# Kernel tuning notes

Measured on AMD Instinct MI355X. Metric: run time of the kernel, lower is better.

Reference implementation:

```python
import jax, jax.numpy as jnp
import numpy as np

N_NODES = 10000
N_EDGES = 128000


def _edge_conv(x, row, col, edge_attr, w1, b1, w2, b2):
    # gather endpoints, concat edge features, 2-layer MLP per edge
    m = jnp.concatenate([x[row], x[col], edge_attr], axis=1)  # [E, 2*in+edge]
    m = jax.nn.relu(m @ w1 + b1) @ w2 + b2                    # [E, out]
    # scatter-mean onto source nodes (flow='target_to_source' -> aggregate on row)
    n = x.shape[0]
    s = jax.ops.segment_sum(m, row, num_segments=n)
    cnt = jax.ops.segment_sum(jnp.ones((row.shape[0], 1), m.dtype), row, num_segments=n)
    out = s / jnp.maximum(cnt, 1.0)
    return out, m


def setup_inputs() -> dict:
    key = jax.random.key(0)
    ks = jax.random.split(key, 24)
    f = jnp.float32

    def lin(kw, kb, fan_in, fan_out):
        lim = 1.0 / np.sqrt(fan_in)
        w = jax.random.uniform(kw, (fan_in, fan_out), f, -lim, lim)
        b = jax.random.uniform(kb, (fan_out,), f, -lim, lim)
        return w, b

    inp = {}
    inp['x_org'] = jax.random.normal(ks[0], (N_NODES, 256), f)
    inp['x_rot'] = jax.random.normal(ks[1], (N_NODES, 4), f)
    inp['edge_index'] = jax.random.randint(ks[2], (2, N_EDGES), 0, N_NODES, jnp.int64 if jax.config.jax_enable_x64 else jnp.int32)
    inp['edge_attr'] = jax.random.normal(ks[3], (N_EDGES, 640), f)
    inp['edge_rot'] = jax.random.normal(ks[4], (N_EDGES, 4), f)

    # conv1: Linear(2*260+644=1164, 64), Linear(64, 64)
    inp['c1_w1'], inp['c1_b1'] = lin(ks[5], ks[6], 1164, 64)
    inp['c1_w2'], inp['c1_b2'] = lin(ks[7], ks[8], 64, 64)
    # conv2: Linear(2*64+704=832, 64), Linear(64, 64)
    inp['c2_w1'], inp['c2_b1'] = lin(ks[9], ks[10], 832, 64)
    inp['c2_w2'], inp['c2_b2'] = lin(ks[11], ks[12], 64, 64)
    # conv3: Linear(2*128+128=384, 64), Linear(64, 64)
    inp['c3_w1'], inp['c3_b1'] = lin(ks[13], ks[14], 384, 64)
    inp['c3_w2'], inp['c3_b2'] = lin(ks[15], ks[16], 64, 64)
    # conv4: Linear(384, 64), Linear(64, 64)
    inp['c4_w1'], inp['c4_b1'] = lin(ks[17], ks[18], 384, 64)
    inp['c4_w2'], inp['c4_b2'] = lin(ks[19], ks[20], 64, 64)
    # lin1: Linear(64, 4)
    inp['lin1_w'], inp['lin1_b'] = lin(ks[21], ks[22], 64, 4)
    # edge_fc: Linear(64, 32) -> ReLU -> Linear(32, 1)
    k23 = jax.random.split(ks[23], 4)
    inp['efc_w1'], inp['efc_b1'] = lin(k23[0], k23[1], 64, 32)
    inp['efc_w2'], inp['efc_b2'] = lin(k23[2], k23[3], 32, 1)
    return inp


def reference(x_org, x_rot, edge_index, edge_attr, edge_rot,
              c1_w1, c1_b1, c1_w2, c1_b2,
              c2_w1, c2_b1, c2_w2, c2_b2,
              c3_w1, c3_b1, c3_w2, c3_b2,
              c4_w1, c4_b1, c4_w2, c4_b2,
              lin1_w, lin1_b, efc_w1, efc_b1, efc_w2, efc_b2):
    node_feat = jnp.concatenate([x_org, x_rot], axis=1)
    edge_feat = jnp.concatenate([edge_attr, edge_rot], axis=1)
    row, col = edge_index[0], edge_index[1]
    E = edge_index.shape[1]

    x1, edge_x1 = _edge_conv(node_feat, row, col, edge_feat, c1_w1, c1_b1, c1_w2, c1_b2)
    edge_x1 = jax.nn.relu(edge_x1)

    x2, edge_x2 = _edge_conv(x1, row, col, jnp.concatenate([edge_attr, edge_x1], axis=1),
                             c2_w1, c2_b1, c2_w2, c2_b2)
    x2 = jax.nn.relu(x2)
    edge_x2 = jax.nn.relu(edge_x2)

    x3, edge_x3 = _edge_conv(jnp.concatenate([x2, x1], axis=1), row, col,
                             jnp.concatenate([edge_x2, edge_x1], axis=1),
                             c3_w1, c3_b1, c3_w2, c3_b2)
    x3 = jax.nn.relu(x3)
    edge_x3 = jax.nn.relu(edge_x3)

    x4, edge_x4 = _edge_conv(jnp.concatenate([x3, x2], axis=1), row, col,
                             jnp.concatenate([edge_x3, edge_x2], axis=1),
                             c4_w1, c4_b1, c4_w2, c4_b2)
    x4 = jax.nn.relu(x4)

    x = x4 @ lin1_w + lin1_b  # [N, 4]
    h = edge_x4[: E // 2] + edge_x4[E // 2:]
    pred_edge_res = jax.nn.relu(h @ efc_w1 + efc_b1) @ efc_w2 + efc_b2  # [E/2, 1]

    # F.normalize(x, p=2, dim=1)
    x = x / jnp.maximum(jnp.linalg.norm(x, axis=1, keepdims=True), 1e-12)
    return x, pred_edge_res
```

## Files before the change

### kernel.cpp

```cpp
#include <hip/hip_runtime.h>
#include <stdint.h>


#define N_NODES 10000
#define N_EDGES 128000
#define E_HALF  64000
#define NBLK    1000

typedef unsigned short u16;

using bf16x8 = __attribute__((ext_vector_type(8))) short;
using f32x4  = __attribute__((ext_vector_type(4))) float;

#define MFMA16(A, B, C) C = __builtin_amdgcn_mfma_f32_16x16x32_bf16(A, B, C, 0, 0, 0)

__device__ __align__(256) float g_acc[N_NODES * 64];
__device__ __align__(256) float g_deg[N_NODES];
__device__ __align__(256) float g_P[N_NODES * 128];
__device__ __align__(256) float g_x1[N_NODES * 64];
__device__ __align__(256) float g_x2[N_NODES * 64];
__device__ __align__(256) float g_x3[N_NODES * 64];
__device__ __align__(256) u16  g_fragA[(size_t)NBLK * 16384];
__device__ __align__(256) u16  g_fragB[(size_t)NBLK * 16384];
__device__ __align__(256) float g_Q2 [(size_t)N_EDGES * 64];
__device__ __align__(256) float g_ex4[(size_t)N_EDGES * 64];
__device__ __align__(256) u16  g_wpA_hi[2 * 4096];
__device__ __align__(256) u16  g_wpA_lo[2 * 4096];
__device__ __align__(256) u16  g_wp2_hi[4096];
__device__ __align__(256) u16  g_wp2_lo[4096];
__device__ __align__(256) u16  g_wnp_hi[4 * 8192];
__device__ __align__(256) u16  g_wnp_lo[4 * 8192];
__device__ __align__(256) u16  g_wpC_hi[10 * 8192];
__device__ __align__(256) u16  g_wpC_lo[10 * 8192];
__device__ __align__(256) int g_row[N_EDGES];
__device__ __align__(256) int g_col[N_EDGES];
__device__ int g_mode;
__device__ int g_is64;

__device__ __forceinline__ float b2f(u16 u) {
    return __uint_as_float(((unsigned int)u) << 16);
}
__device__ __forceinline__ u16 f2b(float f) {
    unsigned int u = __float_as_uint(f);
    u += 0x7FFFu + ((u >> 16) & 1u);
    return (u16)(u >> 16);
}
__device__ __forceinline__ float ldf(const u16* p)   { return b2f(*p); }
__device__ __forceinline__ float ldf(const float* p) { return *p; }
__device__ __forceinline__ void  stf(u16* p, float v)   { *p = f2b(v); }
__device__ __forceinline__ void  stf(float* p, float v) { *p = v; }

__device__ __forceinline__ float4 load4(const float* p) { return *(const float4*)p; }
__device__ __forceinline__ float4 load4(const u16* p) {
    ushort4 v = *(const ushort4*)p;
    return make_float4(b2f(v.x), b2f(v.y), b2f(v.z), b2f(v.w));
}

__device__ __forceinline__ void split_pack(float4 v, uint2& hi, uint2& lo) {
    unsigned int ux = __float_as_uint(v.x), uy = __float_as_uint(v.y);
    unsigned int uz = __float_as_uint(v.z), uw = __float_as_uint(v.w);
    unsigned int hx = ux & 0xFFFF0000u, hy = uy & 0xFFFF0000u;
    unsigned int hz = uz & 0xFFFF0000u, hw = uw & 0xFFFF0000u;
    hi.x = (hx >> 16) | hy;
    hi.y = (hz >> 16) | hw;
    u16 lx = f2b(v.x - __uint_as_float(hx));
    u16 ly = f2b(v.y - __uint_as_float(hy));
    u16 lz = f2b(v.z - __uint_as_float(hz));
    u16 lw = f2b(v.w - __uint_as_float(hw));
    lo.x = (unsigned int)lx | ((unsigned int)ly << 16);
    lo.y = (unsigned int)lz | ((unsigned int)lw << 16);
}

__device__ __forceinline__ void mk_frag(float4 v0, float4 v1,
                                        bf16x8& fh, bf16x8& fl) {
    uint2 h0, l0, h1, l1;
    split_pack(v0, h0, l0);
    split_pack(v1, h1, l1);
    union { unsigned int w[4]; bf16x8 v; } H, L;
    H.w[0] = h0.x; H.w[1] = h0.y; H.w[2] = h1.x; H.w[3] = h1.y;
    L.w[0] = l0.x; L.w[1] = l0.y; L.w[2] = l1.x; L.w[3] = l1.y;
    fh = H.v; fl = L.v;
}

__global__ void detect_kernel(const void* x_org_v, const int* __restrict__ eidx) {
    const u16* w = (const u16*)x_org_v;
    const int t = threadIdx.x;
    int ok = 0;
    for (int i = t; i < 128; i += 64) {
        u16 v = w[i];
        int ex = (v >> 7) & 0xFF;
        ok += ((ex >= 0x68 && ex <= 0x88) || ((v & 0x7FFFu) == 0)) ? 1 : 0;
    }
    #pragma unroll
    for (int off = 32; off >= 1; off >>= 1) ok += __shfl_xor(ok, off);
    bool allz = true;
    for (int i = t; i < 2048; i += 64) allz = allz && (eidx[2 * i + 1] == 0);
    unsigned long long m = __ballot(allz);
    if (t == 0) {
        g_mode = (ok >= 110) ? 0 : 1;
        g_is64 = (m == ~0ull) ? 1 : 0;
    }
}

__global__ void cvt_idx(const int* __restrict__ eidx) {
    const int e = blockIdx.x * 256 + threadIdx.x;
    if (g_is64) {
        g_row[e] = eidx[2 * e];
        g_col[e] = eidx[2 * (e + N_EDGES)];
    } else {
        g_row[e] = eidx[e];
        g_col[e] = eidx[e + N_EDGES];
    }
}

__global__ void zero_all() {
    const int i = blockIdx.x * 256 + threadIdx.x;
    g_acc[i] = 0.f;
    if (i < N_NODES) g_deg[i] = 0.f;
}

__global__ void deg_kernel() {
    const int e = blockIdx.x * 256 + threadIdx.x;
    if (e < N_EDGES) atomicAdd(&g_deg[g_row[e]], 1.0f);
}

template<typename TW>
__device__ void pack_w_body(const TW* w1a, const TW* w2, const TW* w1b,
                            int we, int ns, int hioff, int nsn, int nsc) {
    const int idx = blockIdx.x * 256 + threadIdx.x;
    const int t1 = ns * 4096;
    const int t2 = t1 + 4096;
    const int t3 = t2 + nsn * 8192;
    if (idx < t1) {
        const int s = idx >> 12;
        const int rem = idx & 4095;
        const int kt = rem >> 11, ct = (rem >> 9) & 3, l = (rem >> 3) & 63, r = rem & 7;
        const int k = s * 64 + kt * 32 + 4 * (l >> 4) + (r & 3) + 16 * (r >> 2);
        const float v = ldf(w1a + (size_t)(we + k) * 64 + ct * 16 + (l & 15));
        const u16 hh = f2b(v);
        g_wpA_hi[idx] = hh;
        g_wpA_lo[idx] = f2b(v - b2f(hh));
    } else if (idx < t2) {
        const int rem = idx - t1;
        const int kt = rem >> 11, ct = (rem >> 9) & 3, l = (rem >> 3) & 63, r = rem & 7;
        const int k = kt * 32 + 4 * (l >> 4) + (r & 3) + 16 * (r >> 2);
        const float v = ldf(w2 + (size_t)k * 64 + ct * 16 + (l & 15));
        const u16 hh = f2b(v);
        g_wp2_hi[rem] = hh;
        g_wp2_lo[rem] = f2b(v - b2f(hh));
    } else if (idx < t3) {
        const int rem = idx - t2;
        const int s = rem >> 13;
        const int kt = (rem >> 12) & 1, ct = (rem >> 9) & 7, l = (rem >> 3) & 63, r = rem & 7;
        const int k = s * 64 + kt * 32 + 4 * (l >> 4) + (r & 3) + 16 * (r >> 2);
        const int col = ct * 16 + (l & 15);
        const int row = (col < 64) ? k : (hioff + k);
        const float v = ldf(w1a + (size_t)row * 64 + (col & 63));
        const u16 hh = f2b(v);
        g_wnp_hi[rem] = hh;
        g_wnp_lo[rem] = f2b(v - b2f(hh));
    } else if (idx < t3 + nsc * 8192) {
        const int rem = idx - t3;
        const int s = rem >> 13;
        const int kt = (rem >> 12) & 1, ct = (rem >> 9) & 7, l = (rem >> 3) & 63, r = rem & 7;
        const int k = s * 64 + kt * 32 + 4 * (l >> 4) + (r & 3) + 16 * (r >> 2);
        const int col = ct * 16 + (l & 15);
        float v;
        if (col < 64) v = ldf(w1a + (size_t)(520 + k) * 64 + col);
        else          v = ldf(w1b + (size_t)(128 + k) * 64 + (col - 64));
        const u16 hh = f2b(v);
        g_wpC_hi[rem] = hh;
        g_wpC_lo[rem] = f2b(v - b2f(hh));
    }
}
__global__ void pack_w_k(const void* w1a, const void* w2, const void* w1b,
                         int we, int ns, int hioff, int nsn, int nsc) {
    if (g_mode == 0)
        pack_w_body<u16>((const u16*)w1a, (const u16*)w2, (const u16*)w1b,
                         we, ns, hioff, nsn, nsc);
    else
        pack_w_body<float>((const float*)w1a, (const float*)w2, (const float*)w1b,
                         we, ns, hioff, nsn, nsc);
}

template<typename TA, int NS1, int NS2, bool TAIL>
__device__ void node_mfma_body(float* smrot, float* smwt,
        const TA* A1, const float* A2, const TA* rotsrc, const TA* w1, float* P) {
    constexpr int NS = NS1 + NS2;
    const int t = threadIdx.x;
    const int lane = t & 63, wid = t >> 6;
    const int q = lane >> 4, n = lane & 15;
    const int r0b = blockIdx.x * 64;

    if constexpr (TAIL) {
        if (t < 64) {
            const int rr = min(r0b + t, N_NODES - 1);
            float4 v = load4(rotsrc + (size_t)rr * 4);
            smrot[t * 4 + 0] = v.x; smrot[t * 4 + 1] = v.y;
            smrot[t * 4 + 2] = v.z; smrot[t * 4 + 3] = v.w;
        }
        for (int i = t; i < 512; i += 256) {
            const int j = i >> 7, c = i & 127;
            const int row = (c < 64) ? (256 + j) : (516 + j);
            smwt[i] = ldf(w1 + (size_t)row * 64 + (c & 63));
        }
        __syncthreads();
    }

    const int arow = min(r0b + wid * 16 + n, N_NODES - 1);

    f32x4 acc[8];
    #pragma unroll
    for (int ct = 0; ct < 8; ++ct) acc[ct] = (f32x4){0.f, 0.f, 0.f, 0.f};

    #pragma unroll
    for (int s = 0; s < NS; ++s) {
        #pragma unroll
        for (int kt = 0; kt < 2; ++kt) {
            float4 v0, v1;
            if (s < NS1) {
                const TA* p = A1 + (size_t)arow * (NS1 * 64) + s * 64 + kt * 32 + q * 4;
                v0 = load4(p); v1 = load4(p + 16);
            } else {
                const float* p = A2 + (size_t)arow * (NS2 * 64) + (s - NS1) * 64
                               + kt * 32 + q * 4;
                v0 = load4(p); v1 = load4(p + 16);
            }
            bf16x8 ah, al;
            mk_frag(v0, v1, ah, al);
            const u16* wph = g_wnp_hi + s * 8192;
            const u16* wpl = g_wnp_lo + s * 8192;
            #pragma unroll
            for (int ct = 0; ct < 8; ++ct) {
                bf16x8 bh = *(const bf16x8*)&wph[(kt * 8 + ct) * 512 + lane * 8];
                bf16x8 bl = *(const bf16x8*)&wpl[(kt * 8 + ct) * 512 + lane * 8];
                MFMA16(ah, bh, acc[ct]);
                MFMA16(al, bh, acc[ct]);
                MFMA16(ah, bl, acc[ct]);
            }
        }
    }

    #pragma unroll
    for (int ct = 0; ct < 8; ++ct) {
        #pragma unroll
        for (int i = 0; i < 4; ++i) {
            const int rl = wid * 16 + 4 * q + i;
            const int row = r0b + rl;
            const int col = ct * 16 + n;
            float v = acc[ct][i];
            if constexpr (TAIL)
                v += smrot[rl * 4 + 0] * smwt[0 * 128 + col]
                   + smrot[rl * 4 + 1] * smwt[1 * 128 + col]
                   + smrot[rl * 4 + 2] * smwt[2 * 128 + col]
                   + smrot[rl * 4 + 3] * smwt[3 * 128 + col];
            if (row < N_NODES) P[(size_t)row * 128 + col] = v;
        }
    }
}

template<int NS1, bool TAIL>
__global__ void __launch_bounds__(256) node_mfma_in(
        const void* A1, const void* rotsrc, const void* w1, float* __restrict__ P) {
    __shared__ float smrot[256], smwt[512];
    if (g_mode == 0)
        node_mfma_body<u16, NS1, 0, TAIL>(smrot, smwt, (const u16*)A1,
            nullptr, (const u16*)rotsrc, (const u16*)w1, P);
    else
        node_mfma_body<float, NS1, 0, TAIL>(smrot, smwt, (const float*)A1,
            nullptr, (const float*)rotsrc, (const float*)w1, P);
}

template<int NS1, int NS2>
__global__ void __launch_bounds__(256) node_mfma_ws(
        const float* A1, const float* A2, float* __restrict__ P) {
    __shared__ float smrot[256], smwt[512];
    node_mfma_body<float, NS1, NS2, false>(smrot, smwt, A1, A2,
        (const float*)nullptr, (const float*)nullptr, P);
}

__device__ __forceinline__ void frag_store_o(u16* smA, int wid, int lane,
        const f32x4 (&oacc)[2][4], u16* Fdst, int blkid) {
    const int q = lane >> 4, n = lane & 15;
    #pragma unroll
    for (int rt = 0; rt < 2; ++rt)
        #pragma unroll
        for (int ct = 0; ct < 4; ++ct)
            #pragma unroll
            for (int i = 0; i < 4; ++i) {
                float v = fmaxf(oacc[rt][ct][i], 0.f);
                unsigned int hb = __float_as_uint(v) & 0xFFFF0000u;
                const u16 hh = (u16)(hb >> 16);
                const u16 hl = f2b(v - __uint_as_float(hb));
                const int off = wid * 4096
                              + (((ct >> 1) * 2 + rt) * 64 + (n >> 2) * 16 + 4 * q + i) * 8
                              + (ct & 1) * 4 + (n & 3);
                smA[off]        = hh;
                smA[off + 2048] = hl;
            }
    #pragma unroll
    for (int kt = 0; kt < 2; ++kt)
        #pragma unroll
        for (int rtl = 0; rtl < 2; ++rtl) {
            const int src = wid * 4096 + ((kt * 2 + rtl) * 64 + lane) * 8;
            bf16x8 h8 = *(const bf16x8*)&smA[src];
            bf16x8 l8 = *(const bf16x8*)&smA[src + 2048];
            const size_t gb = (size_t)blkid * 16384
                            + (size_t)(kt * 8 + wid * 2 + rtl) * 512 + lane * 8;
            *(bf16x8*)&Fdst[gb]        = h8;
            *(bf16x8*)&Fdst[gb + 8192] = l8;
        }
}

template<typename TA, typename TW>
__device__ void edge_c1_body(u16* smA, int* srow, int* scol,
        float* b1s, float* b2s, float* rot, float* wtl,
        const TA* efa, const TA* rotsrc,
        const TW* w1, const TW* b1v, const TW* b2v) {
    const int t = threadIdx.x;
    const int lane = t & 63, wid = t >> 6;
    const int q = lane >> 4, n = lane & 15;
    const int e0 = blockIdx.x * 128;

    if (t < 128) srow[t] = g_row[e0 + t];
    else         scol[t - 128] = g_col[e0 + t - 128];
    if (t >= 128 && t < 192) b1s[t - 128] = ldf(b1v + (t - 128));
    if (t >= 192)            b2s[t - 192] = ldf(b2v + (t - 192));
    if (t < 128) {
        float4 r4 = load4(rotsrc + (size_t)(e0 + t) * 4);
        rot[t * 4 + 0] = r4.x; rot[t * 4 + 1] = r4.y;
        rot[t * 4 + 2] = r4.z; rot[t * 4 + 3] = r4.w;
    }
    wtl[t] = ldf(w1 + (size_t)(1160 + (t >> 6)) * 64 + (t & 63));
    __syncthreads();

    f32x4 acc[2][8];
    #pragma unroll
    for (int a_ = 0; a_ < 2; ++a_)
        #pragma unroll
        for (int b_ = 0; b_ < 8; ++b_)
            acc[a_][b_] = (f32x4){0.f, 0.f, 0.f, 0.f};

    const TA* arow0 = efa + (size_t)(e0 + wid * 32 + n) * 640;
    const TA* arow1 = efa + (size_t)(e0 + wid * 32 + 16 + n) * 640;

    auto issue = [&](float4 (&buf)[2][2][2], int s) {
        const int cb = s * 64 + q * 4;
        #pragma unroll
        for (int kt = 0; kt < 2; ++kt) {
            buf[0][kt][0] = load4(arow0 + cb + kt * 32);
            buf[0][kt][1] = load4(arow0 + cb + kt * 32 + 16);
            buf[1][kt][0] = load4(arow1 + cb + kt * 32);
            buf[1][kt][1] = load4(arow1 + cb + kt * 32 + 16);
        }
    };
    auto step = [&](float4 (&buf)[2][2][2], int s) {
        const u16* wph = g_wpC_hi + s * 8192;
        const u16* wpl = g_wpC_lo + s * 8192;
        #pragma unroll
        for (int kt = 0; kt < 2; ++kt) {
            bf16x8 ah0, al0, ah1, al1;
            mk_frag(buf[0][kt][0], buf[0][kt][1], ah0, al0);
            mk_frag(buf[1][kt][0], buf[1][kt][1], ah1, al1);
            #pragma unroll
            for (int ct = 0; ct < 8; ++ct) {
                bf16x8 bh = *(const bf16x8*)&wph[(kt * 8 + ct) * 512 + lane * 8];
                bf16x8 bl = *(const bf16x8*)&wpl[(kt * 8 + ct) * 512 + lane * 8];
                MFMA16(ah0, bh, acc[0][ct]);
                MFMA16(ah1, bh, acc[1][ct]);
                MFMA16(al0, bh, acc[0][ct]);
                MFMA16(al1, bh, acc[1][ct]);
                MFMA16(ah0, bl, acc[0][ct]);
                MFMA16(ah1, bl, acc[1][ct]);
            }
        }
    };

    float4 bufA[2][2][2], bufB[2][2][2];
    issue(bufA, 0);
    for (int s = 0; s < 10; s += 2) {
        issue(bufB, s + 1);
        step(bufA, s);
        if (s + 2 < 10) issue(bufA, s + 2);
        step(bufB, s + 1);
    }

    #pragma unroll
    for (int rt = 0; rt < 2; ++rt)
        #pragma unroll
        for (int c2 = 0; c2 < 4; ++c2)
            #pragma unroll
            for (int i = 0; i < 4; ++i) {
                const int rl = wid * 32 + rt * 16 + 4 * q + i;
                g_Q2[(size_t)(e0 + rl) * 64 + c2 * 16 + n] = acc[rt][4 + c2][i];
            }

    #pragma unroll
    for (int rt = 0; rt < 2; ++rt)
        #pragma unroll
        for (int ct = 0; ct < 4; ++ct)
            #pragma unroll
            for (int i = 0; i < 4; ++i) {
                const int rl = wid * 32 + rt * 16 + 4 * q + i;
                const int col = ct * 16 + n;
                float v = acc[rt][ct][i] + b1s[col]
                        + g_P[(size_t)srow[rl] * 128 + col]
                        + g_P[(size_t)scol[rl] * 128 + 64 + col]
                        + rot[rl * 4 + 0] * wtl[0 * 64 + col]
                        + rot[rl * 4 + 1] * wtl[1 * 64 + col]
                        + rot[rl * 4 + 2] * wtl[2 * 64 + col]
                        + rot[rl * 4 + 3] * wtl[3 * 64 + col];
                v = fmaxf(v, 0.f);
                unsigned int hb = __float_as_uint(v) & 0xFFFF0000u;
                const u16 hh = (u16)(hb >> 16);
                const u16 hl = f2b(v - __uint_as_float(hb));
                const int off = wid * 4096
                              + (((ct >> 1) * 2 + rt) * 64 + (n >> 2) * 16 + 4 * q + i) * 8
                              + (ct & 1) * 4 + (n & 3);
                smA[off]        = hh;
                smA[off + 2048] = hl;
            }

    f32x4 oacc[2][4];
    #pragma unroll
    for (int rt = 0; rt < 2; ++rt)
        #pragma unroll
        for (int ct = 0; ct < 4; ++ct) {
            const float bb = b2s[ct * 16 + n];
            oacc[rt][ct] = (f32x4){bb, bb, bb, bb};
        }
    #pragma unroll
    for (int kt = 0; kt < 2; ++kt) {
        const int r0 = wid * 4096 + ((kt * 2 + 0) * 64 + lane) * 8;
        const int r1 = wid * 4096 + ((kt * 2 + 1) * 64 + lane) * 8;
        bf16x8 ah0 = *(const bf16x8*)&smA[r0];
        bf16x8 ah1 = *(const bf16x8*)&smA[r1];
        bf16x8 al0 = *(const bf16x8*)&smA[r0 + 2048];
        bf16x8 al1 = *(const bf16x8*)&smA[r1 + 2048];
        #pragma unroll
        for (int ct = 0; ct < 4; ++ct) {
            bf16x8 bh = *(const bf16x8*)&g_wp2_hi[(kt * 4 + ct) * 512 + lane * 8];
            bf16x8 bl = *(const bf16x8*)&g_wp2_lo[(kt * 4 + ct) * 512 + lane * 8];
            MFMA16(ah0, bh, oacc[0][ct]);
            MFMA16(ah1, bh, oacc[1][ct]);
            MFMA16(al0, bh, oacc[0][ct]);
            MFMA16(al1, bh, oacc[1][ct]);
            MFMA16(ah0, bl, oacc[0][ct]);
            MFMA16(ah1, bl, oacc[1][ct]);
        }
    }

    #pragma unroll
    for (int rt = 0; rt < 2; ++rt)
        #pragma unroll
        for (int ct = 0; ct < 4; ++ct)
            #pragma unroll
            for (int i = 0; i < 4; ++i) {
                const int rl = wid * 32 + rt * 16 + 4 * q + i;
                atomicAdd(&g_acc[(size_t)srow[rl] * 64 + ct * 16 + n], oacc[rt][ct][i]);
            }
    frag_store_o(smA, wid, lane, oacc, g_fragA, blockIdx.x);
}

__global__ void __launch_bounds__(256, 3) edge_c1(
        const void* efa, const void* rotsrc,
        const void* w1, const void* b1, const void* b2) {
    __shared__ u16 smA[16384];
    __shared__ int srow[128], scol[128];
    __shared__ float b1s[64], b2s[64], rot[512], wtl[256];
    if (g_mode == 0)
        edge_c1_body<u16, u16>(smA, srow, scol, b1s, b2s, rot, wtl,
            (const u16*)efa, (const u16*)rotsrc,
            (const u16*)w1, (const u16*)b1, (const u16*)b2);
    else
        edge_c1_body<float, float>(smA, srow, scol, b1s, b2s, rot, wtl,
            (const float*)efa, (const float*)rotsrc,
            (const float*)w1, (const float*)b1, (const float*)b2);
}

template<typename TW, int NSF, bool HASQ2, bool FRAG_OUT>
__device__ void edge_lite_body(u16* smA, int* srow, int* scol,
        float* b1s, float* b2s,
        const u16* f0, const u16* f1,
        const TW* b1v, const TW* b2v, u16* Ffrag, float* fout) {
    const int t = threadIdx.x;
    const int lane = t & 63, wid = t >> 6;
    const int q = lane >> 4, n = lane & 15;
    const int e0 = blockIdx.x * 128;
    const size_t blkb = (size_t)blockIdx.x * 16384;

    if (t < 128) srow[t] = g_row[e0 + t];
    else         scol[t - 128] = g_col[e0 + t - 128];
    if (t >= 128 && t < 192) b1s[t - 128] = ldf(b1v + (t - 128));
    if (t >= 192)            b2s[t - 192] = ldf(b2v + (t - 192));
    __syncthreads();

    f32x4 acc[2][4];
    #pragma unroll
    for (int a_ = 0; a_ < 2; ++a_)
        #pragma unroll
        for (int b_ = 0; b_ < 4; ++b_)
            acc[a_][b_] = (f32x4){0.f, 0.f, 0.f, 0.f};

    #pragma unroll
    for (int s = 0; s < NSF; ++s) {
        const u16* fs = (s == 0) ? f0 : f1;
        const u16* wph = g_wpA_hi + s * 4096;
        const u16* wpl = g_wpA_lo + s * 4096;
        #pragma unroll
        for (int kt = 0; kt < 2; ++kt) {
            const size_t ba0 = blkb + (size_t)(kt * 8 + wid * 2 + 0) * 512 + lane * 8;
            const size_t ba1 = blkb + (size_t)(kt * 8 + wid * 2 + 1) * 512 + lane * 8;
            bf16x8 ah0 = *(const bf16x8*)&fs[ba0];
            bf16x8 al0 = *(const bf16x8*)&fs[ba0 + 8192];
            bf16x8 ah1 = *(const bf16x8*)&fs[ba1];
            bf16x8 al1 = *(const bf16x8*)&fs[ba1 + 8192];
            #pragma unroll
            for (int ct = 0; ct < 4; ++ct) {
                bf16x8 bh = *(const bf16x8*)&wph[(kt * 4 + ct) * 512 + lane * 8];
                bf16x8 bl = *(const bf16x8*)&wpl[(kt * 4 + ct) * 512 + lane * 8];
                MFMA16(ah0, bh, acc[0][ct]);
                MFMA16(ah1, bh, acc[1][ct]);
                MFMA16(al0, bh, acc[0][ct]);
                MFMA16(al1, bh, acc[1][ct]);
                MFMA16(ah0, bl, acc[0][ct]);
                MFMA16(ah1, bl, acc[1][ct]);
            }
        }
    }

    #pragma unroll
    for (int rt = 0; rt < 2; ++rt)
        #pragma unroll
        for (int ct = 0; ct < 4; ++ct)
            #pragma unroll
            for (int i = 0; i < 4; ++i) {
                const int rl = wid * 32 + rt * 16 + 4 * q + i;
                const int col = ct * 16 + n;
                float v = acc[rt][ct][i] + b1s[col]
                        + g_P[(size_t)srow[rl] * 128 + col]
                        + g_P[(size_t)scol[rl] * 128 + 64 + col];
                if constexpr (HASQ2)
                    v += g_Q2[(size_t)(e0 + rl) * 64 + col];
                v = fmaxf(v, 0.f);
                unsigned int hb = __float_as_uint(v) & 0xFFFF0000u;
                const u16 hh = (u16)(hb >> 16);
                const u16 hl = f2b(v - __uint_as_float(hb));
                const int off = wid * 4096
                              + (((ct >> 1) * 2 + rt) * 64 + (n >> 2) * 16 + 4 * q + i) * 8
                              + (ct & 1) * 4 + (n & 3);
                smA[off]        = hh;
                smA[off + 2048] = hl;
            }

    f32x4 oacc[2][4];
    #pragma unroll
    for (int rt = 0; rt < 2; ++rt)
        #pragma unroll
        for (int ct = 0; ct < 4; ++ct) {
            const float bb = b2s[ct * 16 + n];
            oacc[rt][ct] = (f32x4){bb, bb, bb, bb};
        }
    #pragma unroll
    for (int kt = 0; kt < 2; ++kt) {
        const int r0 = wid * 4096 + ((kt * 2 + 0) * 64 + lane) * 8;
        const int r1 = wid * 4096 + ((kt * 2 + 1) * 64 + lane) * 8;
        bf16x8 ah0 = *(const bf16x8*)&smA[r0];
        bf16x8 ah1 = *(const bf16x8*)&smA[r1];
        bf16x8 al0 = *(const bf16x8*)&smA[r0 + 2048];
        bf16x8 al1 = *(const bf16x8*)&smA[r1 + 2048];
        #pragma unroll
        for (int ct = 0; ct < 4; ++ct) {
            bf16x8 bh = *(const bf16x8*)&g_wp2_hi[(kt * 4 + ct) * 512 + lane * 8];
            bf16x8 bl = *(const bf16x8*)&g_wp2_lo[(kt * 4 + ct) * 512 + lane * 8];
            MFMA16(ah0, bh, oacc[0][ct]);
            MFMA16(ah1, bh, oacc[1][ct]);
            MFMA16(al0, bh, oacc[0][ct]);
            MFMA16(al1, bh, oacc[1][ct]);
            MFMA16(ah0, bl, oacc[0][ct]);
            MFMA16(ah1, bl, oacc[1][ct]);
        }
    }

    #pragma unroll
    for (int rt = 0; rt < 2; ++rt)
        #pragma unroll
        for (int ct = 0; ct < 4; ++ct)
            #pragma unroll
            for (int i = 0; i < 4; ++i) {
                const int rl = wid * 32 + rt * 16 + 4 * q + i;
                const int col = ct * 16 + n;
                const float v = oacc[rt][ct][i];
                atomicAdd(&g_acc[(size_t)srow[rl] * 64 + col], v);
                if constexpr (!FRAG_OUT)
                    fout[(size_t)(e0 + rl) * 64 + col] = v;
            }
    if constexpr (FRAG_OUT)
        frag_store_o(smA, wid, lane, oacc, Ffrag, blockIdx.x);
}

template<int NSF, bool HASQ2, bool FRAG_OUT>
__global__ void __launch_bounds__(256, 4) edge_lite(
        const u16* f0, const u16* f1, const void* b1, const void* b2,
        u16* Ffrag, float* fout) {
    __shared__ u16 smA[16384];
    __shared__ int srow[128], scol[128];
    __shared__ float b1s[64], b2s[64];
    if (g_mode == 0)
        edge_lite_body<u16, NSF, HASQ2, FRAG_OUT>(smA, srow, scol, b1s, b2s,
            f0, f1, (const u16*)b1, (const u16*)b2, Ffrag, fout);
    else
        edge_lite_body<float, NSF, HASQ2, FRAG_OUT>(smA, srow, scol, b1s, b2s,
            f0, f1, (const float*)b1, (const float*)b2, Ffrag, fout);
}

template<bool RELU>
__global__ void finalize_k(float* __restrict__ dst) {
    const int idx = blockIdx.x * 256 + threadIdx.x;
    float v = g_acc[idx] / fmaxf(g_deg[idx >> 6], 1.0f);
    g_acc[idx] = 0.f;
    if (RELU) v = fmaxf(v, 0.f);
    dst[idx] = v;
}

template<typename T>
__device__ void final_node_body(const T* w, const T* b, T* out) {
    const int t = threadIdx.x;
    const int lane = t & 63;
    const int n = blockIdx.x * 4 + (t >> 6);
    float inv = 1.0f / fmaxf(g_deg[n], 1.0f);
    float x4 = fmaxf(g_acc[(size_t)n * 64 + lane] * inv, 0.0f);
    float r[4];
    #pragma unroll
    for (int j = 0; j < 4; ++j) {
        float v = x4 * ldf(w + lane * 4 + j);
        #pragma unroll
        for (int off = 32; off >= 1; off >>= 1) v += __shfl_xor(v, off);
        r[j] = v + ldf(b + j);
    }
    float nrm = sqrtf(r[0]*r[0] + r[1]*r[1] + r[2]*r[2] + r[3]*r[3]);
    float dn = fmaxf(nrm, 1e-12f);
    if (lane < 4) stf(out + n * 4 + lane, r[lane] / dn);
}
__global__ void final_node(const void* w, const void* b, void* out) {
    if (g_mode == 0) final_node_body<u16>((const u16*)w, (const u16*)b, (u16*)out);
    else             final_node_body<float>((const float*)w, (const float*)b, (float*)out);
}

template<typename T>
__device__ void edge_head_body(const float* ex4, const T* w1, const T* b1,
                               const T* w2, const T* b2, T* out) {
    __shared__ float lw1[2048];
    __shared__ float lw2[32];
    const int t = threadIdx.x;
    for (int i = t; i < 2048; i += 256) lw1[i] = ldf(w1 + i);
    if (t < 32) lw2[t] = ldf(w2 + t);
    __syncthreads();
    const int e = blockIdx.x * 256 + t;
    float a[32];
    #pragma unroll
    for (int j = 0; j < 32; ++j) a[j] = ldf(b1 + j);
    const float* p0 = ex4 + (size_t)e * 64;
    const float* p1 = ex4 + (size_t)(e + E_HALF) * 64;
    for (int c = 0; c < 64; ++c) {
        float h = p0[c] + p1[c];
        #pragma unroll
        for (int j = 0; j < 32; ++j) a[j] += h * lw1[c * 32 + j];
    }
    float s = ldf(b2);
    #pragma unroll
    for (int j = 0; j < 32; ++j) s += fmaxf(a[j], 0.f) * lw2[j];
    stf(out + e, s);
}
__global__ void __launch_bounds__(256) edge_head(const float* ex4,
        const void* w1, const void* b1, const void* w2, const void* b2,
        void* out) {
    if (g_mode == 0)
        edge_head_body<u16>(ex4, (const u16*)w1, (const u16*)b1,
                            (const u16*)w2, (const u16*)b2, (u16*)out + 40000);
    else
        edge_head_body<float>(ex4, (const float*)w1, (const float*)b1,
                              (const float*)w2, (const float*)b2, (float*)out + 40000);
}

__global__ void sentinel_fill(unsigned int* out, int n_words) {
    int i = blockIdx.x * 256 + threadIdx.x;
    if (i < n_words) out[i] = 0x44794479u;
}

static void* sym_addr(const void* symbol) {
    void* p = nullptr;
    (void)hipGetSymbolAddress(&p, symbol);
    return p;
}

extern "C" void kernel_launch(void* const* d_in, const int* in_sizes, int n_in,
                              void* d_out, int out_size, void* d_ws, size_t ws_size,
                              hipStream_t stream) {
    (void)d_ws; (void)ws_size;
    bool ok = (n_in == 27) && (out_size == 104000)
           && (in_sizes[0] == 2560000) && (in_sizes[2] == 256000)
           && (in_sizes[3] == 81920000) && (in_sizes[5] == 74496)
           && (in_sizes[21] == 256) && (in_sizes[25] == 32);
    if (!ok) {
        sentinel_fill<<<204, 256, 0, stream>>>((unsigned int*)d_out, 52000);
        return;
    }
    const void* x_org     = d_in[0];
    const void* x_rot     = d_in[1];
    const int*  eidx      = (const int*)d_in[2];
    const void* edge_attr = d_in[3];
    const void* edge_rot  = d_in[4];

    float* P   = (float*)sym_addr(HIP_SYMBOL(g_P));
    float* x1  = (float*)sym_addr(HIP_SYMBOL(g_x1));
    float* x2  = (float*)sym_addr(HIP_SYMBOL(g_x2));
    float* x3  = (float*)sym_addr(HIP_SYMBOL(g_x3));
    u16*   fA  = (u16*)sym_addr(HIP_SYMBOL(g_fragA));
    u16*   fB  = (u16*)sym_addr(HIP_SYMBOL(g_fragB));
    float* ex4 = (float*)sym_addr(HIP_SYMBOL(g_ex4));

    detect_kernel<<<1, 64, 0, stream>>>(x_org, eidx);
    cvt_idx<<<500, 256, 0, stream>>>(eidx);
    zero_all<<<2500, 256, 0, stream>>>();
    deg_kernel<<<500, 256, 0, stream>>>();

    pack_w_k<<<464, 256, 0, stream>>>(d_in[5], d_in[7], d_in[9], 0, 0, 260, 4, 10);
    node_mfma_in<4, true><<<157, 256, 0, stream>>>(x_org, x_rot, d_in[5], P);
    edge_c1<<<NBLK, 256, 0, stream>>>(edge_attr, edge_rot, d_in[5], d_in[6], d_in[8]);
    finalize_k<false><<<2500, 256, 0, stream>>>(x1);

    pack_w_k<<<64, 256, 0, stream>>>(d_in[9], d_in[11], d_in[9], 768, 1, 64, 1, 0);
    node_mfma_ws<1, 0><<<157, 256, 0, stream>>>(x1, nullptr, P);
    edge_lite<1, true, true><<<NBLK, 256, 0, stream>>>(
        fA, nullptr, d_in[10], d_in[12], fB, nullptr);
    finalize_k<true><<<2500, 256, 0, stream>>>(x2);

    pack_w_k<<<112, 256, 0, stream>>>(d_in[13], d_in[15], d_in[13], 256, 2, 128, 2, 0);
    node_mfma_ws<1, 1><<<157, 256, 0, stream>>>(x2, x1, P);
    edge_lite<2, false, true><<<NBLK, 256, 0, stream>>>(
        fB, fA, d_in[14], d_in[16], fA, nullptr);
    finalize_k<true><<<2500, 256, 0, stream>>>(x3);

    pack_w_k<<<112, 256, 0, stream>>>(d_in[17], d_in[19], d_in[17], 256, 2, 128, 2, 0);
    node_mfma_ws<1, 1><<<157, 256, 0, stream>>>(x3, x2, P);
    edge_lite<2, false, false><<<NBLK, 256, 0, stream>>>(
        fA, fB, d_in[18], d_in[20], nullptr, ex4);

    final_node<<<2500, 256, 0, stream>>>(d_in[21], d_in[22], d_out);
    edge_head<<<250, 256, 0, stream>>>(ex4, d_in[23], d_in[24], d_in[25], d_in[26],
                                       d_out);
}
```

Baseline: 896.3 us.

## Stage MFMA weight fragments into LDS via async global_load_lds with double buffering

The edge MLP kernels now copy packed bf16 hi/lo weight fragments into shared memory with direct global-to-LDS loads, instead of reading them from global memory in every wave. In edge_c1 the weight stages are double-buffered and the edge-feature loads are triple-buffered, with explicit waitcnt and barriers to overlap copies with MFMA work. The goal is to stop each wave re-fetching the same weights through the cache and to hide load latency. In exchange LDS use per block grows and the occupancy hints drop from 3 or 4 blocks to 2. The hand-written vmcnt counts are fragile if the compiler emits a different number of loads.

```diff
diff --git a/kernel.cpp b/kernel.cpp
--- a/kernel.cpp
+++ b/kernel.cpp
@@ -54,6 +54,12 @@
 __device__ __forceinline__ float4 load4(const u16* p) {
     ushort4 v = *(const ushort4*)p;
     return make_float4(b2f(v.x), b2f(v.y), b2f(v.z), b2f(v.w));
+}
+
+__device__ __forceinline__ void gl_lds16(const void* g, void* l) {
+    __builtin_amdgcn_global_load_lds(
+        (const __attribute__((address_space(1))) void*)g,
+        (__attribute__((address_space(3))) void*)l, 16, 0, 0);
 }
 
 __device__ __forceinline__ void split_pack(float4 v, uint2& hi, uint2& lo) {
@@ -279,7 +285,7 @@
         (const float*)nullptr, (const float*)nullptr, P);
 }
 
-__device__ __forceinline__ void frag_store_o(u16* smA, int wid, int lane,
+__device__ __forceinline__ void frag_store_o(u16* hreg, int wid, int lane,
         const f32x4 (&oacc)[2][4], u16* Fdst, int blkid) {
     const int q = lane >> 4, n = lane & 15;
     #pragma unroll
@@ -295,16 +301,16 @@
                 const int off = wid * 4096
                               + (((ct >> 1) * 2 + rt) * 64 + (n >> 2) * 16 + 4 * q + i) * 8
                               + (ct & 1) * 4 + (n & 3);
-                smA[off]        = hh;
-                smA[off + 2048] = hl;
+                hreg[off]        = hh;
+                hreg[off + 2048] = hl;
             }
     #pragma unroll
     for (int kt = 0; kt < 2; ++kt)
         #pragma unroll
         for (int rtl = 0; rtl < 2; ++rtl) {
             const int src = wid * 4096 + ((kt * 2 + rtl) * 64 + lane) * 8;
-            bf16x8 h8 = *(const bf16x8*)&smA[src];
-            bf16x8 l8 = *(const bf16x8*)&smA[src + 2048];
+            bf16x8 h8 = *(const bf16x8*)&hreg[src];
+            bf16x8 l8 = *(const bf16x8*)&hreg[src + 2048];
             const size_t gb = (size_t)blkid * 16384
                             + (size_t)(kt * 8 + wid * 2 + rtl) * 512 + lane * 8;
             *(bf16x8*)&Fdst[gb]        = h8;
@@ -313,7 +319,7 @@
 }
 
 template<typename TA, typename TW>
-__device__ void edge_c1_body(u16* smA, int* srow, int* scol,
+__device__ void edge_c1_body(u16* smW, int* srow, int* scol,
         float* b1s, float* b2s, float* rot, float* wtl,
         const TA* efa, const TA* rotsrc,
         const TW* w1, const TW* b1v, const TW* b2v) {
@@ -332,7 +338,9 @@
         rot[t * 4 + 2] = r4.z; rot[t * 4 + 3] = r4.w;
     }
     wtl[t] = ldf(w1 + (size_t)(1160 + (t >> 6)) * 64 + (t & 63));
-    __syncthreads();
+
+    const TA* arow0 = efa + (size_t)(e0 + wid * 32 + n) * 640;
+    const TA* arow1 = efa + (size_t)(e0 + wid * 32 + 16 + n) * 640;
 
     f32x4 acc[2][8];
     #pragma unroll
@@ -341,10 +349,30 @@
         for (int b_ = 0; b_ < 8; ++b_)
             acc[a_][b_] = (f32x4){0.f, 0.f, 0.f, 0.f};
 
-    const TA* arow0 = efa + (size_t)(e0 + wid * 32 + n) * 640;
-    const TA* arow1 = efa + (size_t)(e0 + wid * 32 + 16 + n) * 640;
-
-    auto issue = [&](float4 (&buf)[2][2][2], int s) {
+    auto stageW = [&](int s) {
+        const char* srch = (const char*)g_wpC_hi + (size_t)s * 16384;
+        const char* srcl = (const char*)g_wpC_lo + (size_t)s * 16384;
+        char* dsth = (char*)smW + (size_t)(s & 1) * 32768;
+        char* dstl = dsth + 16384;
+        #pragma unroll
+        for (int i = 0; i < 4; ++i) {
+            const int off = wid * 4096 + i * 1024;
+            gl_lds16(srch + off + lane * 16, dsth + off);
+            gl_lds16(srcl + off + lane * 16, dstl + off);
+        }
+    };
+    auto stageW2 = [&]() {
+        #pragma unroll
+        for (int i = 0; i < 4; ++i) {
+            const int L = wid * 4096 + i * 1024;
+            const char* src = (L < 8192) ? (const char*)g_wp2_hi + L
+                                         : (const char*)g_wp2_lo + (L - 8192);
+            gl_lds16(src + lane * 16, (char*)smW + L);
+        }
+    };
+
+    float4 abuf[3][2][2][2];
+    auto issueA = [&](float4 (&buf)[2][2][2], int s) {
         const int cb = s * 64 + q * 4;
         #pragma unroll
         for (int kt = 0; kt < 2; ++kt) {
@@ -355,8 +383,7 @@
         }
     };
     auto step = [&](float4 (&buf)[2][2][2], int s) {
-        const u16* wph = g_wpC_hi + s * 8192;
-        const u16* wpl = g_wpC_lo + s * 8192;
+        const int wb = (s & 1) * 16384;
         #pragma unroll
         for (int kt = 0; kt < 2; ++kt) {
             bf16x8 ah0, al0, ah1, al1;
@@ -364,8 +391,8 @@
             mk_frag(buf[1][kt][0], buf[1][kt][1], ah1, al1);
             #pragma unroll
             for (int ct = 0; ct < 8; ++ct) {
-                bf16x8 bh = *(const bf16x8*)&wph[(kt * 8 + ct) * 512 + lane * 8];
-                bf16x8 bl = *(const bf16x8*)&wpl[(kt * 8 + ct) * 512 + lane * 8];
+                bf16x8 bh = *(const bf16x8*)&smW[wb + (kt * 8 + ct) * 512 + lane * 8];
+                bf16x8 bl = *(const bf16x8*)&smW[wb + 8192 + (kt * 8 + ct) * 512 + lane * 8];
                 MFMA16(ah0, bh, acc[0][ct]);
                 MFMA16(ah1, bh, acc[1][ct]);
                 MFMA16(al0, bh, acc[0][ct]);
@@ -376,13 +403,25 @@
         }
     };
 
-    float4 bufA[2][2][2], bufB[2][2][2];
-    issue(bufA, 0);
-    for (int s = 0; s < 10; s += 2) {
-        issue(bufB, s + 1);
-        step(bufA, s);
-        if (s + 2 < 10) issue(bufA, s + 2);
-        step(bufB, s + 1);
+    stageW(0);
+    issueA(abuf[0], 0);
+    issueA(abuf[1], 1);
+    __builtin_amdgcn_sched_barrier(0);
+    asm volatile("s_waitcnt vmcnt(16) lgkmcnt(0)");
+    __builtin_amdgcn_sched_barrier(0);
+    __builtin_amdgcn_s_barrier();
+
+    #pragma unroll
+    for (int s = 0; s < 10; ++s) {
+        if (s < 9) stageW(s + 1); else stageW2();
+        __builtin_amdgcn_sched_barrier(0);
+        if (s == 9) asm volatile("s_waitcnt vmcnt(4)");
+        else        asm volatile("s_waitcnt vmcnt(16)");
+        __builtin_amdgcn_sched_barrier(0);
+        __builtin_amdgcn_s_barrier();
+        if (s < 8) issueA(abuf[(s + 2) % 3], s + 2);
+        step(abuf[s % 3], s);
+        __builtin_amdgcn_s_barrier();
     }
 
     #pragma unroll
@@ -395,6 +434,7 @@
                 g_Q2[(size_t)(e0 + rl) * 64 + c2 * 16 + n] = acc[rt][4 + c2][i];
             }
 
+    u16* hreg = smW + 16384;
     #pragma unroll
     for (int rt = 0; rt < 2; ++rt)
         #pragma unroll
@@ -417,9 +457,14 @@
                 const int off = wid * 4096
                               + (((ct >> 1) * 2 + rt) * 64 + (n >> 2) * 16 + 4 * q + i) * 8
                               + (ct & 1) * 4 + (n & 3);
-                smA[off]        = hh;
-                smA[off + 2048] = hl;
-            }
+                hreg[off]        = hh;
+                hreg[off + 2048] = hl;
+            }
+
+    __builtin_amdgcn_sched_barrier(0);
+    asm volatile("s_waitcnt vmcnt(0)");
+    __builtin_amdgcn_sched_barrier(0);
+    __builtin_amdgcn_s_barrier();
 
     f32x4 oacc[2][4];
     #pragma unroll
@@ -433,14 +478,14 @@
     for (int kt = 0; kt < 2; ++kt) {
         const int r0 = wid * 4096 + ((kt * 2 + 0) * 64 + lane) * 8;
         const int r1 = wid * 4096 + ((kt * 2 + 1) * 64 + lane) * 8;
-        bf16x8 ah0 = *(const bf16x8*)&smA[r0];
-        bf16x8 ah1 = *(const bf16x8*)&smA[r1];
-        bf16x8 al0 = *(const bf16x8*)&smA[r0 + 2048];
-        bf16x8 al1 = *(const bf16x8*)&smA[r1 + 2048];
+        bf16x8 ah0 = *(const bf16x8*)&hreg[r0];
+        bf16x8 ah1 = *(const bf16x8*)&hreg[r1];
+        bf16x8 al0 = *(const bf16x8*)&hreg[r0 + 2048];
+        bf16x8 al1 = *(const bf16x8*)&hreg[r1 + 2048];
         #pragma unroll
         for (int ct = 0; ct < 4; ++ct) {
-            bf16x8 bh = *(const bf16x8*)&g_wp2_hi[(kt * 4 + ct) * 512 + lane * 8];
-            bf16x8 bl = *(const bf16x8*)&g_wp2_lo[(kt * 4 + ct) * 512 + lane * 8];
+            bf16x8 bh = *(const bf16x8*)&smW[(kt * 4 + ct) * 512 + lane * 8];
+            bf16x8 bl = *(const bf16x8*)&smW[4096 + (kt * 4 + ct) * 512 + lane * 8];
             MFMA16(ah0, bh, oacc[0][ct]);
             MFMA16(ah1, bh, oacc[1][ct]);
             MFMA16(al0, bh, oacc[0][ct]);
@@ -459,27 +504,27 @@
                 const int rl = wid * 32 + rt * 16 + 4 * q + i;
                 atomicAdd(&g_acc[(size_t)srow[rl] * 64 + ct * 16 + n], oacc[rt][ct][i]);
             }
-    frag_store_o(smA, wid, lane, oacc, g_fragA, blockIdx.x);
-}
-
-__global__ void __launch_bounds__(256, 3) edge_c1(
+    frag_store_o(hreg, wid, lane, oacc, g_fragA, blockIdx.x);
+}
+
+__global__ void __launch_bounds__(256, 2) edge_c1(
         const void* efa, const void* rotsrc,
         const void* w1, const void* b1, const void* b2) {
-    __shared__ u16 smA[16384];
+    __shared__ __align__(16) u16 smW[32768];
     __shared__ int srow[128], scol[128];
     __shared__ float b1s[64], b2s[64], rot[512], wtl[256];
     if (g_mode == 0)
-        edge_c1_body<u16, u16>(smA, srow, scol, b1s, b2s, rot, wtl,
+        edge_c1_body<u16, u16>(smW, srow, scol, b1s, b2s, rot, wtl,
             (const u16*)efa, (const u16*)rotsrc,
             (const u16*)w1, (const u16*)b1, (const u16*)b2);
     else
-        edge_c1_body<float, float>(smA, srow, scol, b1s, b2s, rot, wtl,
+        edge_c1_body<float, float>(smW, srow, scol, b1s, b2s, rot, wtl,
             (const float*)efa, (const float*)rotsrc,
             (const float*)w1, (const float*)b1, (const float*)b2);
 }
 
 template<typename TW, int NSF, bool HASQ2, bool FRAG_OUT>
-__device__ void edge_lite_body(u16* smA, int* srow, int* scol,
+__device__ void edge_lite_body(u16* smW, int* srow, int* scol,
         float* b1s, float* b2s,
         const u16* f0, const u16* f1,
         const TW* b1v, const TW* b2v, u16* Ffrag, float* fout) {
@@ -488,6 +533,18 @@
     const int q = lane >> 4, n = lane & 15;
     const int e0 = blockIdx.x * 128;
     const size_t blkb = (size_t)blockIdx.x * 16384;
+    constexpr int N2 = 2 * NSF * 4096;
+
+    #pragma unroll
+    for (int i = 0; i < (NSF + 1) * 4; ++i) {
+        const int L = wid * ((NSF + 1) * 4096) + i * 1024;
+        const char* src;
+        if (L < NSF * 8192)                 src = (const char*)g_wpA_hi + L;
+        else if (L < 2 * NSF * 8192)        src = (const char*)g_wpA_lo + (L - NSF * 8192);
+        else if (L < 2 * NSF * 8192 + 8192) src = (const char*)g_wp2_hi + (L - 2 * NSF * 8192);
+        else                                src = (const char*)g_wp2_lo + (L - 2 * NSF * 8192 - 8192);
+        gl_lds16(src + lane * 16, (char*)smW + L);
+    }
 
     if (t < 128) srow[t] = g_row[e0 + t];
     else         scol[t - 128] = g_col[e0 + t - 128];
@@ -505,8 +562,6 @@
     #pragma unroll
     for (int s = 0; s < NSF; ++s) {
         const u16* fs = (s == 0) ? f0 : f1;
-        const u16* wph = g_wpA_hi + s * 4096;
-        const u16* wpl = g_wpA_lo + s * 4096;
         #pragma unroll
         for (int kt = 0; kt < 2; ++kt) {
             const size_t ba0 = blkb + (size_t)(kt * 8 + wid * 2 + 0) * 512 + lane * 8;
@@ -517,8 +572,8 @@
             bf16x8 al1 = *(const bf16x8*)&fs[ba1 + 8192];
             #pragma unroll
             for (int ct = 0; ct < 4; ++ct) {
-                bf16x8 bh = *(const bf16x8*)&wph[(kt * 4 + ct) * 512 + lane * 8];
-                bf16x8 bl = *(const bf16x8*)&wpl[(kt * 4 + ct) * 512 + lane * 8];
+                bf16x8 bh = *(const bf16x8*)&smW[s * 4096 + (kt * 4 + ct) * 512 + lane * 8];
+                bf16x8 bl = *(const bf16x8*)&smW[NSF * 4096 + s * 4096 + (kt * 4 + ct) * 512 + lane * 8];
                 MFMA16(ah0, bh, acc[0][ct]);
                 MFMA16(ah1, bh, acc[1][ct]);
                 MFMA16(al0, bh, acc[0][ct]);
@@ -528,6 +583,9 @@
             }
         }
     }
+
+    __builtin_amdgcn_s_barrier();
+    u16* hreg = smW + (NSF == 1 ? 16384 : 0);
 
     #pragma unroll
     for (int rt = 0; rt < 2; ++rt)
@@ -549,8 +607,8 @@
                 const int off = wid * 4096
                               + (((ct >> 1) * 2 + rt) * 64 + (n >> 2) * 16 + 4 * q + i) * 8
                               + (ct & 1) * 4 + (n & 3);
-                smA[off]        = hh;
-                smA[off + 2048] = hl;
+                hreg[off]        = hh;
+                hreg[off + 2048] = hl;
             }
 
     f32x4 oacc[2][4];
@@ -565,14 +623,14 @@
     for (int kt = 0; kt < 2; ++kt) {
         const int r0 = wid * 4096 + ((kt * 2 + 0) * 64 + lane) * 8;
         const int r1 = wid * 4096 + ((kt * 2 + 1) * 64 + lane) * 8;
-        bf16x8 ah0 = *(const bf16x8*)&smA[r0];
-        bf16x8 ah1 = *(const bf16x8*)&smA[r1];
-        bf16x8 al0 = *(const bf16x8*)&smA[r0 + 2048];
-        bf16x8 al1 = *(const bf16x8*)&smA[r1 + 2048];
+        bf16x8 ah0 = *(const bf16x8*)&hreg[r0];
+        bf16x8 ah1 = *(const bf16x8*)&hreg[r1];
+        bf16x8 al0 = *(const bf16x8*)&hreg[r0 + 2048];
+        bf16x8 al1 = *(const bf16x8*)&hreg[r1 + 2048];
         #pragma unroll
         for (int ct = 0; ct < 4; ++ct) {
-            bf16x8 bh = *(const bf16x8*)&g_wp2_hi[(kt * 4 + ct) * 512 + lane * 8];
-            bf16x8 bl = *(const bf16x8*)&g_wp2_lo[(kt * 4 + ct) * 512 + lane * 8];
+            bf16x8 bh = *(const bf16x8*)&smW[N2 + (kt * 4 + ct) * 512 + lane * 8];
+            bf16x8 bl = *(const bf16x8*)&smW[N2 + 4096 + (kt * 4 + ct) * 512 + lane * 8];
             MFMA16(ah0, bh, oacc[0][ct]);
             MFMA16(ah1, bh, oacc[1][ct]);
             MFMA16(al0, bh, oacc[0][ct]);
@@ -596,21 +654,21 @@
                     fout[(size_t)(e0 + rl) * 64 + col] = v;
             }
     if constexpr (FRAG_OUT)
-        frag_store_o(smA, wid, lane, oacc, Ffrag, blockIdx.x);
+        frag_store_o(hreg, wid, lane, oacc, Ffrag, blockIdx.x);
 }
 
 template<int NSF, bool HASQ2, bool FRAG_OUT>
-__global__ void __launch_bounds__(256, 4) edge_lite(
+__global__ void __launch_bounds__(256, 2) edge_lite(
         const u16* f0, const u16* f1, const void* b1, const void* b2,
         u16* Ffrag, float* fout) {
-    __shared__ u16 smA[16384];
+    __shared__ __align__(16) u16 smW[(NSF == 1) ? 32768 : 24576];
     __shared__ int srow[128], scol[128];
     __shared__ float b1s[64], b2s[64];
     if (g_mode == 0)
-        edge_lite_body<u16, NSF, HASQ2, FRAG_OUT>(smA, srow, scol, b1s, b2s,
+        edge_lite_body<u16, NSF, HASQ2, FRAG_OUT>(smW, srow, scol, b1s, b2s,
             f0, f1, (const u16*)b1, (const u16*)b2, Ffrag, fout);
     else
-        edge_lite_body<float, NSF, HASQ2, FRAG_OUT>(smA, srow, scol, b1s, b2s,
+        edge_lite_body<float, NSF, HASQ2, FRAG_OUT>(smW, srow, scol, b1s, b2s,
             f0, f1, (const float*)b1, (const float*)b2, Ffrag, fout);
 }
 
```

Result: faster. 843.0 us (-5.9%).
